# Performance work log

Hardware: AMD Instinct MI355X
Metric: run time of the kernel (lower is better)

## Reference

```python
import jax, jax.numpy as jnp
import numpy as np

B, T, C, H = 2, 2048, 2048, 16
HD = C // H  # 128


def setup_inputs() -> dict:
    key = jax.random.key(0)
    k1, k2, k3 = jax.random.split(key, 3)
    x = jax.random.normal(k1, (B, T, C), jnp.float32)
    qkv_w = jax.random.normal(k2, (3 * C, C), jnp.float32) / np.float32(np.sqrt(C))
    proj_w = jax.random.normal(k3, (C, C), jnp.float32) / np.float32(np.sqrt(C))
    past = jnp.zeros((B, H, 2, T, HD), jnp.float32)  # KV cache: [B,H,2,max_seq,hd]
    return {"x": x, "qkv_w": qkv_w, "proj_w": proj_w, "past": past, "past_len": 0}


def reference(x, qkv_w, proj_w, past, past_len):
    Bx, Tx, Cx = x.shape
    hd = Cx // H
    # qkv projection (no bias), then split heads: [B,T,3C] -> [B,T,3,H,hd] -> [B,H,T,hd] each
    qkv = jnp.einsum('btc,dc->btd', x, qkv_w).reshape(Bx, Tx, 3, H, hd)
    q = jnp.transpose(qkv[:, :, 0], (0, 2, 1, 3))
    k = jnp.transpose(qkv[:, :, 1], (0, 2, 1, 3))
    v = jnp.transpose(qkv[:, :, 2], (0, 2, 1, 3))
    # KV-cache write (functional scatter) then read back the valid prefix
    past = past.at[:, :, 0, past_len:past_len + Tx].set(k)
    past = past.at[:, :, 1, past_len:past_len + Tx].set(v)
    k = past[:, :, 0, :past_len + Tx]
    v = past[:, :, 1, :past_len + Tx]
    S = past_len + Tx
    scale = np.float32(1.0 / np.sqrt(hd))
    scores = jnp.einsum('bhqd,bhkd->bhqk', q, k) * scale  # [B,H,T,S]
    if Tx > 1:  # is_causal=T>1 in the torch module (past_len=0 on this path)
        mask = jnp.arange(S)[None, :] <= (jnp.arange(Tx)[:, None] + past_len)
        scores = jnp.where(mask, scores, jnp.float32(-jnp.inf))
    attn = jax.nn.softmax(scores, axis=-1)
    out = jnp.einsum('bhqk,bhkd->bhqd', attn, v)  # [B,H,T,hd]
    out = jnp.transpose(out, (0, 2, 1, 3)).reshape(Bx, Tx, Cx)
    return jnp.einsum('btc,dc->btd', out, proj_w)
```

## Files before the change

### kernel.cpp

```cpp
#include <hip/hip_runtime.h>

typedef __bf16 bf16x8 __attribute__((ext_vector_type(8)));
typedef float f32x4 __attribute__((ext_vector_type(4)));
typedef unsigned short u16x8 __attribute__((ext_vector_type(8)));
typedef unsigned short u16x4 __attribute__((ext_vector_type(4)));

__device__ __forceinline__ unsigned short f2bf(float f) {
  return __builtin_bit_cast(unsigned short, (__bf16)f);
}

__device__ __forceinline__ void gload16(const void* g, void* l) {
  __builtin_amdgcn_global_load_lds((const __attribute__((address_space(1))) unsigned int*)g,
                                   (__attribute__((address_space(3))) unsigned int*)l,
                                   16, 0, 0);
}

template <int N>
__device__ __forceinline__ float rormax(float x) {
  int r = __builtin_amdgcn_update_dpp(0, __builtin_bit_cast(int, x), 0x120 + N, 0xF, 0xF, true);
  return fmaxf(x, __builtin_bit_cast(float, r));
}
template <int N>
__device__ __forceinline__ float rorsum(float x) {
  int r = __builtin_amdgcn_update_dpp(0, __builtin_bit_cast(int, x), 0x120 + N, 0xF, 0xF, true);
  return x + __builtin_bit_cast(float, r);
}
__device__ __forceinline__ float red16max(float x) {
  x = rormax<8>(x); x = rormax<4>(x); x = rormax<2>(x); return rormax<1>(x);
}
__device__ __forceinline__ float red16sum(float x) {
  x = rorsum<8>(x); x = rorsum<4>(x); x = rorsum<2>(x); return rorsum<1>(x);
}

__global__ __launch_bounds__(256)
void cvt3_f32_bf16(const float* __restrict__ s0, unsigned short* __restrict__ d0, int n0,
                   const float* __restrict__ s1, unsigned short* __restrict__ d1, int n1,
                   const float* __restrict__ s2, unsigned short* __restrict__ d2)
{
  int blk = blockIdx.x;
  const float* s; unsigned short* d;
  if (blk < n0)            { s = s0; d = d0; }
  else if (blk < n0 + n1)  { s = s1; d = d1; blk -= n0; }
  else                     { s = s2; d = d2; blk -= n0 + n1; }
  const size_t e = ((size_t)blk * 256 + threadIdx.x) * 8;
  const float4 a = *(const float4*)(s + e);
  const float4 b = *(const float4*)(s + e + 4);
  u16x8 v;
  v[0] = f2bf(a.x); v[1] = f2bf(a.y); v[2] = f2bf(a.z); v[3] = f2bf(a.w);
  v[4] = f2bf(b.x); v[5] = f2bf(b.y); v[6] = f2bf(b.z); v[7] = f2bf(b.w);
  *(u16x8*)(d + e) = v;
}

#define SA(buf, half, kt)                                                       \
  { gload16(Ag + (size_t)((half)*128 + srow8) * K + (kt)*64 + scol,             \
            As + (buf)*32768 + (half)*16384 + wid*1024);                        \
    gload16(Ag + (size_t)((half)*128 + 64 + srow8) * K + (kt)*64 + scol,        \
            As + (buf)*32768 + (half)*16384 + 8192 + wid*1024); }

#define SB(buf, u, kt)                                                          \
  { gload16(Bg + (size_t)((u)*64 + srow8) * K + (kt)*64 + scol,                 \
            Bs + (buf)*24576 + (u)*8192 + wid*1024); }

#define LA(buf, ih)                                                             \
  { _Pragma("unroll") for (int i = 0; i < 4; ++i) {                             \
      const int ro = (buf)*32768 + arow + ((ih)*64 + i*16)*128;                 \
      af[i][0] = *(const bf16x8*)(As + ro + cbs0);                              \
      af[i][1] = *(const bf16x8*)(As + ro + cbs1); } }

#define LB2(buf)                                                                \
  { _Pragma("unroll") for (int j = 0; j < 2; ++j) {                             \
      const int ro = (buf)*24576 + brow + j*2048;                               \
      B2[j][0] = *(const bf16x8*)(Bs + ro + cbs0);                              \
      B2[j][1] = *(const bf16x8*)(Bs + ro + cbs1); } }

#define LB1(buf)                                                                \
  { const int ro = (buf)*24576 + brow + 4096;                                   \
    B1[0] = *(const bf16x8*)(Bs + ro + cbs0);                                   \
    B1[1] = *(const bf16x8*)(Bs + ro + cbs1); }

#define M2(ih)                                                                  \
  { _Pragma("unroll") for (int i = 0; i < 4; ++i)                               \
    _Pragma("unroll") for (int j = 0; j < 2; ++j)                               \
    _Pragma("unroll") for (int kk = 0; kk < 2; ++kk)                            \
      acc[(ih)*4+i][j] = __builtin_amdgcn_mfma_f32_16x16x32_bf16(               \
          af[i][kk], B2[j][kk], acc[(ih)*4+i][j], 0, 0, 0); }

#define M1(ih)                                                                  \
  { _Pragma("unroll") for (int i = 0; i < 4; ++i)                               \
    _Pragma("unroll") for (int kk = 0; kk < 2; ++kk)                            \
      acc[(ih)*4+i][2] = __builtin_amdgcn_mfma_f32_16x16x32_bf16(               \
          af[i][kk], B1[kk], acc[(ih)*4+i][2], 0, 0, 0); }

#define BAR1_12() { asm volatile("s_waitcnt lgkmcnt(8)" ::: "memory");          \
                    __builtin_amdgcn_s_barrier();                               \
                    asm volatile("s_waitcnt lgkmcnt(0)" ::: "memory");          \
                    __builtin_amdgcn_sched_barrier(0);                          \
                    __builtin_amdgcn_s_setprio(1); }
#define BAR1()    { __builtin_amdgcn_s_barrier();                               \
                    asm volatile("s_waitcnt lgkmcnt(0)" ::: "memory");          \
                    __builtin_amdgcn_sched_barrier(0);                          \
                    __builtin_amdgcn_s_setprio(1); }
#define BAR2()    { __builtin_amdgcn_s_setprio(0); __builtin_amdgcn_s_barrier(); }
#define BAR2V3()  { __builtin_amdgcn_s_setprio(0);                              \
                    asm volatile("s_waitcnt vmcnt(3)" ::: "memory");            \
                    __builtin_amdgcn_s_barrier(); }

__global__ __launch_bounds__(512, 1)
void gemm_n192(const unsigned short* __restrict__ Ap, const unsigned short* __restrict__ Bp,
               unsigned short* __restrict__ QKout, unsigned short* __restrict__ vT,
               int M, int N, int K)
{
  extern __shared__ __align__(16) char smem[];
  char* const As = smem;
  char* const Bs = smem + 65536;
  const int tid = threadIdx.x;
  const int wid = tid >> 6, lane = tid & 63;
  const int wm = wid >> 2, wn = wid & 3;
  const int lg = lane >> 4, lr = lane & 15;

  const int gx = gridDim.x;
  const int nwg = gx * (int)gridDim.y;
  int bid = (int)blockIdx.y * gx + (int)blockIdx.x;
  bid = (bid & 7) * (nwg >> 3) + (bid >> 3);
  const int m0 = (bid / gx) * 256, n0 = (bid % gx) * 192;

  const int srow8 = wid * 8 + (lane >> 3);
  const int scol  = (((lane & 7) ^ (lane >> 3)) << 3);
  const unsigned short* const Ag = Ap + (size_t)m0 * K;
  const unsigned short* const Bg = Bp + (size_t)n0 * K;

  const int cbs0 = (lg * 16) ^ ((lr & 7) << 4);
  const int cbs1 = (64 + lg * 16) ^ ((lr & 7) << 4);
  const int arow = (wm * 128 + lr) * 128;
  const int brow = (wn * 48 + lr) * 128;

  const f32x4 z4 = {0.f, 0.f, 0.f, 0.f};
  f32x4 acc[8][3];
#pragma unroll
  for (int i = 0; i < 8; ++i)
#pragma unroll
    for (int j = 0; j < 3; ++j) acc[i][j] = z4;

  const int NKT = K >> 6;
  bf16x8 af[4][2], B2[2][2], B1[2];

  SA(0, 0, 0); SA(0, 1, 0);
  SB(0, 0, 0); SB(0, 1, 0); SB(0, 2, 0);
  SB(1, 0, 1); SB(1, 1, 1); SB(1, 2, 1);
  asm volatile("s_waitcnt vmcnt(3)" ::: "memory");
  __builtin_amdgcn_s_barrier();

  for (int it = 0; it < (NKT >> 1); ++it) {
    const int t1  = 2 * it + 1;
    const int t0n = (2 * it + 2 < NKT) ? 2 * it + 2 : NKT - 1;
    const int t1n = (t1 + 2 < NKT) ? t1 + 2 : NKT - 1;

    LA(0, 0); LB2(0); SA(1, 0, t1);
    BAR1_12(); M2(0); BAR2();
    LB1(0); SA(1, 1, t1);
    BAR1(); M1(0); BAR2();
    LA(0, 1); SB(0, 0, t0n); SB(0, 1, t0n);
    BAR1(); M2(1); BAR2();
    SB(0, 2, t0n);
    BAR1(); M1(1); BAR2V3();
    LA(1, 0); LB2(1); SA(0, 0, t0n);
    BAR1_12(); M2(0); BAR2();
    LB1(1); SA(0, 1, t0n);
    BAR1(); M1(0); BAR2();
    LA(1, 1); SB(1, 0, t1n); SB(1, 1, t1n);
    BAR1(); M2(1); BAR2();
    SB(1, 2, t1n);
    BAR1(); M1(1); BAR2V3();
  }
  asm volatile("s_waitcnt vmcnt(0)" ::: "memory");

  const int d4 = 4096 - n0;
  const int vlo = d4 <= 0 ? 0 : (d4 >= 192 ? 192 : d4);

#pragma unroll
  for (int i = 0; i < 8; ++i)
#pragma unroll
    for (int j = 0; j < 3; ++j) {
      const int clb = wn * 48 + j * 16;
      if (clb < vlo) {
        const int row0 = m0 + wm * 128 + i * 16 + lg * 4;
#pragma unroll
        for (int r = 0; r < 4; ++r)
          QKout[(size_t)(row0 + r) * 4096 + n0 + clb + lr] = f2bf(acc[i][j][r]);
      }
    }

  if (vlo < 192) {
    char* const Lt = smem;
    __syncthreads();
#pragma unroll
    for (int i = 0; i < 8; ++i)
#pragma unroll
      for (int j = 0; j < 3; ++j) {
        const int clb = wn * 48 + j * 16;
        if (clb >= vlo) {
          const int cl = clb + lr - vlo;
          const int t  = wm * 128 + i * 16 + lg * 4;
          u16x4 pack;
          pack[0] = f2bf(acc[i][j][0]); pack[1] = f2bf(acc[i][j][1]);
          pack[2] = f2bf(acc[i][j][2]); pack[3] = f2bf(acc[i][j][3]);
          *(u16x4*)(Lt + cl * 512 + ((t * 2) ^ ((cl & 7) << 4))) = pack;
        }
      }
    __syncthreads();
    const int ncl = 192 - vlo;
    const int cbase = n0 + vlo - 4096;
    const int bb = m0 >> 11, t0g = m0 & 2047;
    for (int chunk = tid; chunk < ncl * 32; chunk += 512) {
      const int cl = chunk >> 5, tt = (chunk & 31) * 8;
      u16x8 v = *(const u16x8*)(Lt + cl * 512 + ((tt * 2) ^ ((cl & 7) << 4)));
      const int gc = cbase + cl;
      *(u16x8*)(vT + ((size_t)(bb * 16 + (gc >> 7)) * 128 + (gc & 127)) * 2048 + t0g + tt) = v;
    }
  }
}

template <bool OUTBF16>
__global__ __launch_bounds__(256, 2)
void gemm_bt16(const unsigned short* __restrict__ Ap, const unsigned short* __restrict__ Bp,
               void* __restrict__ Outp, int M, int N, int K)
{
  __shared__ __align__(16) char smA[128 * 128];
  __shared__ __align__(16) char smB[128 * 128];
  const int tid = threadIdx.x;
  const int wid = tid >> 6, lane = tid & 63;
  const int wr = wid >> 1, wc = wid & 1;
  const int lg = lane >> 4, lr = lane & 15;

  const int gx = gridDim.x;
  const int nwg = gx * gridDim.y;
  int bid = blockIdx.y * gx + blockIdx.x;
  bid = (bid & 7) * (nwg >> 3) + (bid >> 3);
  const int m0 = (bid / gx) * 128, n0 = (bid % gx) * 128;

  const int srow = wid * 8 + (lane >> 3);
  const int scol = (((lane & 7) ^ (lane >> 3)) << 3);
  const int lbase = wid * 1024;

  const f32x4 z4 = {0.f, 0.f, 0.f, 0.f};
  f32x4 acc[4][4];
#pragma unroll
  for (int i = 0; i < 4; ++i)
#pragma unroll
    for (int j = 0; j < 4; ++j) acc[i][j] = z4;

  for (int k0 = 0; k0 < K; k0 += 64) {
    __syncthreads();
#pragma unroll
    for (int c = 0; c < 4; ++c) {
      const int row = c * 32 + srow;
      gload16(Ap + (size_t)(m0 + row) * K + k0 + scol, smA + c * 4096 + lbase);
      gload16(Bp + (size_t)(n0 + row) * K + k0 + scol, smB + c * 4096 + lbase);
    }
    __syncthreads();
#pragma unroll
    for (int kk = 0; kk < 2; ++kk) {
      const int cb = (kk * 32 + lg * 8) * 2;
      bf16x8 a4[4], b4[4];
#pragma unroll
      for (int i = 0; i < 4; ++i) {
        const int row = wr * 64 + i * 16 + lr;
        a4[i] = *(const bf16x8*)(smA + row * 128 + (cb ^ ((row & 7) << 4)));
      }
#pragma unroll
      for (int j = 0; j < 4; ++j) {
        const int row = wc * 64 + j * 16 + lr;
        b4[j] = *(const bf16x8*)(smB + row * 128 + (cb ^ ((row & 7) << 4)));
      }
#pragma unroll
      for (int i = 0; i < 4; ++i)
#pragma unroll
        for (int j = 0; j < 4; ++j)
          acc[i][j] = __builtin_amdgcn_mfma_f32_16x16x32_bf16(a4[i], b4[j], acc[i][j], 0, 0, 0);
    }
  }
#pragma unroll
  for (int i = 0; i < 4; ++i)
#pragma unroll
    for (int j = 0; j < 4; ++j)
#pragma unroll
      for (int r = 0; r < 4; ++r) {
        const int row = m0 + wr * 64 + i * 16 + lg * 4 + r;
        const int col = n0 + wc * 64 + j * 16 + lr;
        const float val = acc[i][j][r];
        if (OUTBF16) ((unsigned short*)Outp)[(size_t)row * N + col] = f2bf(val);
        else         ((float*)Outp)[(size_t)row * N + col] = val;
      }
}

__global__ __launch_bounds__(256, 2)
void attn_fwd(const unsigned short* __restrict__ qk, const unsigned short* __restrict__ vT,
              unsigned short* __restrict__ outp)
{
  constexpr int T = 2048, ROWS = 4096;
  const int blk = blockIdx.x;
  const int qt = 31 - (blk >> 5);
  const int bh = blk & 31;
  const int b = bh >> 4, h = bh & 15;
  const int q0 = qt * 64;
  const int tid = threadIdx.x;
  const int wid = tid >> 6, lane = tid & 63;
  const int lg = lane >> 4, lr = lane & 15;

  __shared__ __align__(16) char Ks[128 * 256];
  __shared__ __align__(16) char Vt[128 * 256];
  __shared__ __align__(16) char Ps[64 * 256];

  const int srow = wid * 4 + (lane >> 4);
  const int scol = (((lane & 15) ^ (srow & 7)) << 3);

  const size_t qrow = (size_t)(b * T + q0 + wid * 16 + lr) * ROWS + h * 128;
  bf16x8 qf[4];
#pragma unroll
  for (int kd = 0; kd < 4; ++kd)
    qf[kd] = __builtin_bit_cast(bf16x8, *(const u16x8*)(qk + qrow + kd * 32 + lg * 8));

  const f32x4 z4 = {0.f, 0.f, 0.f, 0.f};
  f32x4 oacc[8];
#pragma unroll
  for (int jj = 0; jj < 8; ++jj) oacc[jj] = z4;
  float mrow[4] = {-1e30f, -1e30f, -1e30f, -1e30f};
  float lsum[4] = {0.f, 0.f, 0.f, 0.f};
  const float scale2 = 0.12751745f;

  const int nt = (qt >> 1) + 1;
  for (int kt = 0; kt < nt; ++kt) {
    __syncthreads();
#pragma unroll
    for (int c = 0; c < 8; ++c) {
      gload16(qk + (size_t)(b * T + kt * 128 + c * 16 + srow) * ROWS + 2048 + h * 128 + scol,
              Ks + c * 4096 + wid * 1024);
      gload16(vT + ((size_t)bh * 128 + c * 16 + srow) * 2048 + kt * 128 + scol,
              Vt + c * 4096 + wid * 1024);
    }
    asm volatile("s_waitcnt vmcnt(0)" ::: "memory");
    __syncthreads();

    f32x4 sf[8];
#pragma unroll
    for (int j = 0; j < 8; ++j) sf[j] = z4;
    __builtin_amdgcn_s_setprio(1);
#pragma unroll
    for (int kd = 0; kd < 4; ++kd) {
      const int cb = (kd * 32 + lg * 8) * 2;
#pragma unroll
      for (int j = 0; j < 8; ++j) {
        const int row = j * 16 + lr;
        bf16x8 kf = *(const bf16x8*)(Ks + row * 256 + (cb ^ ((row & 7) << 4)));
        sf[j] = __builtin_amdgcn_mfma_f32_16x16x32_bf16(qf[kd], kf, sf[j], 0, 0, 0);
      }
    }
    __builtin_amdgcn_s_setprio(0);

    const bool diag = (kt == nt - 1);
#pragma unroll
    for (int j = 0; j < 8; ++j)
#pragma unroll
      for (int r = 0; r < 4; ++r) {
        float s = sf[j][r] * scale2;
        const int key = kt * 128 + j * 16 + lr;
        const int qi  = q0 + wid * 16 + lg * 4 + r;
        if (diag && key > qi) s = -1e30f;
        sf[j][r] = s;
      }
    float pm[4];
#pragma unroll
    for (int r = 0; r < 4; ++r) {
      float m0 = fmaxf(fmaxf(sf[0][r], sf[1][r]), fmaxf(sf[2][r], sf[3][r]));
      float m1 = fmaxf(fmaxf(sf[4][r], sf[5][r]), fmaxf(sf[6][r], sf[7][r]));
      pm[r] = red16max(fmaxf(m0, m1));
    }
    const float growth = fmaxf(fmaxf(pm[0] - mrow[0], pm[1] - mrow[1]),
                               fmaxf(pm[2] - mrow[2], pm[3] - mrow[3]));
    const bool resc = !__all(growth <= 11.5f);
    float alpha[4];
    if (resc) {
#pragma unroll
      for (int r = 0; r < 4; ++r) {
        const float mn = fmaxf(mrow[r], pm[r]);
        alpha[r] = exp2f(mrow[r] - mn);
        mrow[r] = mn;
      }
    }
    float rs[4] = {0.f, 0.f, 0.f, 0.f};
#pragma unroll
    for (int j = 0; j < 8; ++j)
#pragma unroll
      for (int r = 0; r < 4; ++r) {
        const float p = exp2f(sf[j][r] - mrow[r]);
        sf[j][r] = p;
        rs[r] += p;
      }
    if (resc) {
#pragma unroll
      for (int r = 0; r < 4; ++r) lsum[r] = lsum[r] * alpha[r] + red16sum(rs[r]);
    } else {
#pragma unroll
      for (int r = 0; r < 4; ++r) lsum[r] += red16sum(rs[r]);
    }

#pragma unroll
    for (int j = 0; j < 8; ++j)
#pragma unroll
      for (int r = 0; r < 4; ++r) {
        const int prow = wid * 16 + lg * 4 + r;
        const int pcol = j * 16 + lr;
        *(unsigned short*)(Ps + prow * 256 + ((pcol * 2) ^ ((prow & 7) << 4))) = f2bf(sf[j][r]);
      }
    if (resc) {
#pragma unroll
      for (int jj = 0; jj < 8; ++jj)
#pragma unroll
        for (int r = 0; r < 4; ++r) oacc[jj][r] *= alpha[r];
    }
    asm volatile("s_waitcnt lgkmcnt(0)" ::: "memory");
    __builtin_amdgcn_sched_barrier(0);

    __builtin_amdgcn_s_setprio(1);
#pragma unroll
    for (int kk = 0; kk < 4; ++kk) {
      const int prow = wid * 16 + lr;
      const int pcb = (kk * 32 + lg * 8) * 2;
      bf16x8 pf = *(const bf16x8*)(Ps + prow * 256 + (pcb ^ ((prow & 7) << 4)));
#pragma unroll
      for (int jj = 0; jj < 8; ++jj) {
        const int vrow = jj * 16 + lr;
        bf16x8 vf = *(const bf16x8*)(Vt + vrow * 256 + (pcb ^ ((vrow & 7) << 4)));
        oacc[jj] = __builtin_amdgcn_mfma_f32_16x16x32_bf16(pf, vf, oacc[jj], 0, 0, 0);
      }
    }
    __builtin_amdgcn_s_setprio(0);
  }

#pragma unroll
  for (int jj = 0; jj < 8; ++jj)
#pragma unroll
    for (int r = 0; r < 4; ++r) {
      const int q = q0 + wid * 16 + lg * 4 + r;
      const int col = h * 128 + jj * 16 + lr;
      const float o = oacc[jj][r] / lsum[r];
      outp[(size_t)(b * T + q) * 2048 + col] = f2bf(o);
    }
}

extern "C" void kernel_launch(void* const* d_in, const int* in_sizes, int n_in,
                              void* d_out, int out_size, void* d_ws, size_t ws_size,
                              hipStream_t stream) {
  (void)in_sizes; (void)n_in; (void)out_size; (void)ws_size;
  const float* x     = (const float*)d_in[0];
  const float* qkvw  = (const float*)d_in[1];
  const float* projw = (const float*)d_in[2];

  unsigned short* qkb    = (unsigned short*)d_ws;
  unsigned short* vT     = qkb + (size_t)4096 * 4096;
  unsigned short* attnb  = qkb + (size_t)4096 * 6144;
  unsigned short* xb     = attnb  + (size_t)4096 * 2048;
  unsigned short* qkvwb  = xb     + (size_t)4096 * 2048;
  unsigned short* projwb = qkvwb  + (size_t)6144 * 2048;
  float* out = (float*)d_out;

  static bool attr_set = false;
  if (!attr_set) {
    hipFuncSetAttribute((const void*)gemm_n192,
                        hipFuncAttributeMaxDynamicSharedMemorySize, 114688);
    attr_set = true;
  }

  cvt3_f32_bf16<<<4096 + 6144 + 2048, 256, 0, stream>>>(
      x, xb, 4096, qkvw, qkvwb, 6144, projw, projwb);
  gemm_n192<<<dim3(6144 / 192, 4096 / 256), 512, 114688, stream>>>(
      xb, qkvwb, qkb, vT, 4096, 6144, 2048);
  attn_fwd<<<1024, 256, 0, stream>>>(qkb, vT, attnb);
  gemm_bt16<false><<<dim3(2048 / 128, 4096 / 128), 256, 0, stream>>>(
      attnb, projwb, out, 4096, 2048, 2048);
}
```

Baseline: 246.4 us.

## Replace output projection GEMM with double-buffered 128x256 pipelined kernel

The output projection GEMM moves from a single-buffered 128x128 tile with 256 threads to a 128x256 tile with 512 threads. The new kernel double-buffers A and B in dynamic LDS and interleaves global-to-LDS loads with MFMA phases, using split barriers and partial vmcnt waits. This is meant to hide global load latency and raise operand reuse per block. It cuts the grid to 256 blocks, which may underfill the GPU, and it relies on BAR1/BAR2 macros presumably defined in the hidden part of the file.

```diff
diff --git a/kernel.cpp b/kernel.cpp
--- a/kernel.cpp
+++ b/kernel.cpp
@@ -220,27 +220,68 @@
   }
 }
 
-template <bool OUTBF16>
-__global__ __launch_bounds__(256, 2)
-void gemm_bt16(const unsigned short* __restrict__ Ap, const unsigned short* __restrict__ Bp,
-               void* __restrict__ Outp, int M, int N, int K)
+#define STGA3(buf, kt)                                                          \
+  { gload16(Ag + (size_t)(srow8) * K + (kt)*64 + scol,                          \
+            As + (buf)*16384 + wid*1024);                                       \
+    gload16(Ag + (size_t)(64 + srow8) * K + (kt)*64 + scol,                     \
+            As + (buf)*16384 + 8192 + wid*1024); }
+
+#define STGB3(buf, half, kt)                                                    \
+  { gload16(Bg + (size_t)((half)*128 + srow8) * K + (kt)*64 + scol,             \
+            Bs + (buf)*32768 + (half)*16384 + wid*1024);                        \
+    gload16(Bg + (size_t)((half)*128 + 64 + srow8) * K + (kt)*64 + scol,        \
+            Bs + (buf)*32768 + (half)*16384 + 8192 + wid*1024); }
+
+#define LDA3(buf, ih)                                                           \
+  { _Pragma("unroll") for (int i2 = 0; i2 < 2; ++i2) {                          \
+      const int ro = (buf)*16384 + arow + ((ih)*32 + i2*16)*128;                \
+      af[i2][0] = *(const bf16x8*)(As + ro + cbs0);                             \
+      af[i2][1] = *(const bf16x8*)(As + ro + cbs1); } }
+
+#define LDB3(buf, jh, BF)                                                       \
+  { _Pragma("unroll") for (int j = 0; j < 2; ++j) {                             \
+      const int ro = (buf)*32768 + brow + (((jh)*2 + j)*16)*128;                \
+      BF[j][0] = *(const bf16x8*)(Bs + ro + cbs0);                              \
+      BF[j][1] = *(const bf16x8*)(Bs + ro + cbs1); } }
+
+#define MM3(ih, jh, BF)                                                         \
+  { _Pragma("unroll") for (int i2 = 0; i2 < 2; ++i2)                            \
+    _Pragma("unroll") for (int j = 0; j < 2; ++j)                               \
+    _Pragma("unroll") for (int kk = 0; kk < 2; ++kk)                            \
+      acc[(ih)*2+i2][(jh)*2+j] = __builtin_amdgcn_mfma_f32_16x16x32_bf16(       \
+          af[i2][kk], BF[j][kk], acc[(ih)*2+i2][(jh)*2+j], 0, 0, 0); }
+
+#define BAR2V4()  { __builtin_amdgcn_s_setprio(0);                              \
+                    asm volatile("s_waitcnt vmcnt(4)" ::: "memory");            \
+                    __builtin_amdgcn_s_barrier(); }
+
+__global__ __launch_bounds__(512, 1)
+void gemm128x256(const unsigned short* __restrict__ Ap, const unsigned short* __restrict__ Bp,
+                 float* __restrict__ Outp, int M, int N, int K)
 {
-  __shared__ __align__(16) char smA[128 * 128];
-  __shared__ __align__(16) char smB[128 * 128];
+  extern __shared__ __align__(16) char smem[];
+  char* const As = smem;
+  char* const Bs = smem + 32768;
   const int tid = threadIdx.x;
   const int wid = tid >> 6, lane = tid & 63;
-  const int wr = wid >> 1, wc = wid & 1;
+  const int wm = wid >> 2, wn = wid & 3;
   const int lg = lane >> 4, lr = lane & 15;
 
   const int gx = gridDim.x;
-  const int nwg = gx * gridDim.y;
-  int bid = blockIdx.y * gx + blockIdx.x;
+  const int nwg = gx * (int)gridDim.y;
+  int bid = (int)blockIdx.y * gx + (int)blockIdx.x;
   bid = (bid & 7) * (nwg >> 3) + (bid >> 3);
-  const int m0 = (bid / gx) * 128, n0 = (bid % gx) * 128;
-
-  const int srow = wid * 8 + (lane >> 3);
-  const int scol = (((lane & 7) ^ (lane >> 3)) << 3);
-  const int lbase = wid * 1024;
+  const int m0 = (bid / gx) * 128, n0 = (bid % gx) * 256;
+
+  const int srow8 = wid * 8 + (lane >> 3);
+  const int scol  = (((lane & 7) ^ (lane >> 3)) << 3);
+  const unsigned short* const Ag = Ap + (size_t)m0 * K;
+  const unsigned short* const Bg = Bp + (size_t)n0 * K;
+
+  const int cbs0 = (lg * 16) ^ ((lr & 7) << 4);
+  const int cbs1 = (64 + lg * 16) ^ ((lr & 7) << 4);
+  const int arow = (wm * 64 + lr) * 128;
+  const int brow = (wn * 64 + lr) * 128;
 
   const f32x4 z4 = {0.f, 0.f, 0.f, 0.f};
   f32x4 acc[4][4];
@@ -249,47 +290,47 @@
 #pragma unroll
     for (int j = 0; j < 4; ++j) acc[i][j] = z4;
 
-  for (int k0 = 0; k0 < K; k0 += 64) {
-    __syncthreads();
-#pragma unroll
-    for (int c = 0; c < 4; ++c) {
-      const int row = c * 32 + srow;
-      gload16(Ap + (size_t)(m0 + row) * K + k0 + scol, smA + c * 4096 + lbase);
-      gload16(Bp + (size_t)(n0 + row) * K + k0 + scol, smB + c * 4096 + lbase);
-    }
-    __syncthreads();
-#pragma unroll
-    for (int kk = 0; kk < 2; ++kk) {
-      const int cb = (kk * 32 + lg * 8) * 2;
-      bf16x8 a4[4], b4[4];
-#pragma unroll
-      for (int i = 0; i < 4; ++i) {
-        const int row = wr * 64 + i * 16 + lr;
-        a4[i] = *(const bf16x8*)(smA + row * 128 + (cb ^ ((row & 7) << 4)));
-      }
-#pragma unroll
-      for (int j = 0; j < 4; ++j) {
-        const int row = wc * 64 + j * 16 + lr;
-        b4[j] = *(const bf16x8*)(smB + row * 128 + (cb ^ ((row & 7) << 4)));
-      }
-#pragma unroll
-      for (int i = 0; i < 4; ++i)
-#pragma unroll
-        for (int j = 0; j < 4; ++j)
-          acc[i][j] = __builtin_amdgcn_mfma_f32_16x16x32_bf16(a4[i], b4[j], acc[i][j], 0, 0, 0);
-    }
+  const int NKT = K >> 6;
+  bf16x8 af[2][2], bf01[2][2], bf23[2][2];
+
+  STGA3(0, 0); STGB3(0, 0, 0); STGB3(0, 1, 0);
+  STGB3(1, 0, 1); STGB3(1, 1, 1);
+  asm volatile("s_waitcnt vmcnt(4)" ::: "memory");
+  __builtin_amdgcn_s_barrier();
+
+  for (int it = 0; it < (NKT >> 1); ++it) {
+    const int t1  = 2 * it + 1;
+    const int t0n = (2 * it + 2 < NKT) ? 2 * it + 2 : NKT - 1;
+    const int t1n = (t1 + 2 < NKT) ? t1 + 2 : NKT - 1;
+
+    LDA3(0, 0); LDB3(0, 0, bf01); STGA3(1, t1);
+    BAR1(); MM3(0, 0, bf01); BAR2();
+    LDB3(0, 1, bf23);
+    BAR1(); MM3(0, 1, bf23); BAR2();
+    LDA3(0, 1); STGB3(0, 0, t0n);
+    BAR1(); MM3(1, 0, bf01); BAR2();
+    STGB3(0, 1, t0n);
+    BAR1(); MM3(1, 1, bf23); BAR2V4();
+    LDA3(1, 0); LDB3(1, 0, bf01); STGA3(0, t0n);
+    BAR1(); MM3(0, 0, bf01); BAR2();
+    LDB3(1, 1, bf23);
+    BAR1(); MM3(0, 1, bf23); BAR2();
+    LDA3(1, 1); STGB3(1, 0, t1n);
+    BAR1(); MM3(1, 0, bf01); BAR2();
+    STGB3(1, 1, t1n);
+    BAR1(); MM3(1, 1, bf23); BAR2V4();
   }
+  asm volatile("s_waitcnt vmcnt(0)" ::: "memory");
+
 #pragma unroll
   for (int i = 0; i < 4; ++i)
 #pragma unroll
     for (int j = 0; j < 4; ++j)
 #pragma unroll
       for (int r = 0; r < 4; ++r) {
-        const int row = m0 + wr * 64 + i * 16 + lg * 4 + r;
-        const int col = n0 + wc * 64 + j * 16 + lr;
-        const float val = acc[i][j][r];
-        if (OUTBF16) ((unsigned short*)Outp)[(size_t)row * N + col] = f2bf(val);
-        else         ((float*)Outp)[(size_t)row * N + col] = val;
+        const int row = m0 + wm * 64 + i * 16 + lg * 4 + r;
+        const int col = n0 + wn * 64 + j * 16 + lr;
+        Outp[(size_t)row * N + col] = acc[i][j][r];
       }
 }
 
@@ -468,6 +509,8 @@
   if (!attr_set) {
     hipFuncSetAttribute((const void*)gemm_n192,
                         hipFuncAttributeMaxDynamicSharedMemorySize, 114688);
+    hipFuncSetAttribute((const void*)gemm128x256,
+                        hipFuncAttributeMaxDynamicSharedMemorySize, 98304);
     attr_set = true;
   }
 
@@ -476,6 +519,6 @@
   gemm_n192<<<dim3(6144 / 192, 4096 / 256), 512, 114688, stream>>>(
       xb, qkvwb, qkb, vT, 4096, 6144, 2048);
   attn_fwd<<<1024, 256, 0, stream>>>(qkb, vT, attnb);
-  gemm_bt16<false><<<dim3(2048 / 128, 4096 / 128), 256, 0, stream>>>(
+  gemm128x256<<<dim3(2048 / 256, 4096 / 128), 512, 98304, stream>>>(
       attnb, projwb, out, 4096, 2048, 2048);
 }
```

New measurement: 236.9 us, median of 17. 3.9% less time.
